# Kernel optimization log

Measured on AMD Instinct MI355X. Metric: run time of the kernel, lower is better.

Reference implementation:

```python
import jax, jax.numpy as jnp
import numpy as np

H, DK, DV = 16, 64, 64


def _ln(x, w, b, eps=1e-5):
    mu = x.mean(-1, keepdims=True)
    var = ((x - mu) ** 2).mean(-1, keepdims=True)
    return (x - mu) * jax.lax.rsqrt(var + eps) * w + b


def setup_inputs() -> dict:
    key = jax.random.key(0)
    ks = jax.random.split(key, 8)
    B, L, D = 4, 1024, 1024
    q = jax.random.normal(ks[0], (B, L, D), jnp.float32)
    k = jax.random.normal(ks[1], (B, L, D), jnp.float32)
    v = jax.random.normal(ks[2], (B, L, D), jnp.float32)
    mask = jax.random.randint(ks[3], (B, L, L), 0, 2).astype(jnp.int32)
    diag_mask = jnp.zeros((1,), jnp.int32)  # unused by the original attention math
    sq = np.sqrt(2.0 / (D + DK)).astype(np.float32)
    sv = np.sqrt(2.0 / (D + DV)).astype(np.float32)
    wq = jax.random.normal(ks[4], (H * DK, D), jnp.float32) * sq
    wk = jax.random.normal(ks[5], (H * DK, D), jnp.float32) * sq
    wv = jax.random.normal(ks[6], (H * DV, D), jnp.float32) * sv
    wfc = jax.random.normal(ks[7], (D, H * DV), jnp.float32) * 0.02
    ones, zeros = jnp.ones((D,), jnp.float32), jnp.zeros((D,), jnp.float32)
    return {
        'q': q, 'k': k, 'v': v, 'diag_mask': diag_mask, 'mask': mask,
        'ln1_w': ones, 'ln1_b': zeros, 'ln2_w': ones, 'ln2_b': zeros,
        'ln3_w': ones, 'ln3_b': zeros, 'wq': wq, 'wk': wk, 'wv': wv, 'wfc': wfc,
    }


def reference(q, k, v, diag_mask, mask, ln1_w, ln1_b, ln2_w, ln2_b, ln3_w, ln3_b, wq, wk, wv, wfc):
    B, Lq, _ = q.shape
    Lk = k.shape[1]
    qn = _ln(q, ln1_w, ln1_b)
    kn = _ln(k, ln2_w, ln2_b)
    vn = _ln(v, ln3_w, ln3_b)
    qh = (qn @ wq.T).reshape(B, Lq, H, DK)
    kh = (kn @ wk.T).reshape(B, Lk, H, DK)
    vh = (vn @ wv.T).reshape(B, Lk, H, DV)
    # head-major layout matches torch's permute(2,0,1,3).view(-1,...)
    logits = jnp.einsum('bqhd,bkhd->hbqk', qh, kh) / jnp.float32(DK ** 0.5)
    m = mask[None] != 0  # broadcast mask over heads, [1,B,Lq,Lk]
    logits = jnp.where(m, jnp.float32(-1e32), logits)  # memory_efficient mask_fill
    p = jax.nn.softmax(logits, axis=-1)
    p = p * (~m)  # post-softmax zeroing, as in masked_softmax
    ctx = jnp.einsum('hbqk,bkhd->bqhd', p, vh).reshape(B, Lq, H * DV)
    dynamic = ctx @ wfc.T  # fc1: single bias-free Linear, no tanh/dropout
    attn = p.reshape(H * B, Lq, Lk)
    return dynamic, attn
```

## Files before the change

### kernel.cpp

```cpp
#include <hip/hip_runtime.h>
#include <hip/hip_bf16.h>

#define B_ 4
#define L_ 1024
#define D_ 1024
#define H_ 16
#define NROWS_ (B_ * L_)

typedef __attribute__((ext_vector_type(8))) short short8;
typedef __attribute__((ext_vector_type(4))) float f32x4;

__device__ __forceinline__ ushort f2bf(float f) {
    union { float f; uint u; } x; x.f = f;
    return (ushort)((x.u + 0x7fffu + ((x.u >> 16) & 1u)) >> 16);
}
__device__ __forceinline__ float bf2f(ushort u) {
    union { uint u; float f; } x; x.u = (uint)u << 16; return x.f;
}
__device__ __forceinline__ void gl_lds16(const void* g, void* l) {
    __builtin_amdgcn_global_load_lds(
        (const __attribute__((address_space(1))) uint*)(uintptr_t)g,
        (__attribute__((address_space(3))) uint*)(uintptr_t)l, 16, 0, 0);
}

#define EXP2C 0.1803368801111244f

__global__ __launch_bounds__(256) void lnwcvt_kernel(
    const float* __restrict__ q, const float* __restrict__ k, const float* __restrict__ v,
    const float* __restrict__ ln1w, const float* __restrict__ ln1b,
    const float* __restrict__ ln2w, const float* __restrict__ ln2b,
    const float* __restrict__ ln3w, const float* __restrict__ ln3b,
    ushort* __restrict__ qn, ushort* __restrict__ kn, ushort* __restrict__ vn,
    const float* __restrict__ wq, const float* __restrict__ wk,
    const float* __restrict__ wv, const float* __restrict__ wfc,
    ushort* __restrict__ wqb, ushort* __restrict__ wkb,
    ushort* __restrict__ wvb, ushort* __restrict__ wfcb)
{
    const int bid = blockIdx.x, t = threadIdx.x;
    if (bid >= 12288) {
        const int wbid = bid - 12288;
        const int which = wbid >> 10;
        const float* src = which == 0 ? wq : which == 1 ? wk : which == 2 ? wv : wfc;
        ushort* dst      = which == 0 ? wqb : which == 1 ? wkb : which == 2 ? wvb : wfcb;
        const size_t i = (size_t)(wbid & 1023) * 256 + t;
        const float4 f = ((const float4*)src)[i];
        ushort4 o; o.x = f2bf(f.x); o.y = f2bf(f.y); o.z = f2bf(f.z); o.w = f2bf(f.w);
        ((ushort4*)dst)[i] = o;
        return;
    }
    const int which = bid >> 12, row = bid & 4095;
    const float *x, *lw, *lb; ushort* out;
    if (which == 0)      { x = q; lw = ln1w; lb = ln1b; out = qn; }
    else if (which == 1) { x = k; lw = ln2w; lb = ln2b; out = kn; }
    else                 { x = v; lw = ln3w; lb = ln3b; out = vn; }
    x += (size_t)row * D_; out += (size_t)row * D_;
    const float4 t4 = ((const float4*)x)[t];
    float s  = t4.x + t4.y + t4.z + t4.w;
    float s2 = t4.x*t4.x + t4.y*t4.y + t4.z*t4.z + t4.w*t4.w;
    #pragma unroll
    for (int off = 1; off < 64; off <<= 1) {
        s  += __shfl_xor(s,  off, 64);
        s2 += __shfl_xor(s2, off, 64);
    }
    __shared__ float red[8];
    __shared__ float mr[2];
    const int wid = t >> 6;
    if ((t & 63) == 0) { red[wid*2] = s; red[wid*2+1] = s2; }
    __syncthreads();
    if (t == 0) {
        s  = red[0] + red[2] + red[4] + red[6];
        s2 = red[1] + red[3] + red[5] + red[7];
        const float mean = s * (1.0f/(float)D_);
        const float var  = s2 * (1.0f/(float)D_) - mean*mean;
        mr[0] = mean; mr[1] = rsqrtf(var + 1e-5f);
    }
    __syncthreads();
    const float mean = mr[0], rstd = mr[1];
    const float4 w4 = ((const float4*)lw)[t];
    const float4 b4 = ((const float4*)lb)[t];
    ushort4 o;
    o.x = f2bf((t4.x - mean)*rstd*w4.x + b4.x);
    o.y = f2bf((t4.y - mean)*rstd*w4.y + b4.y);
    o.z = f2bf((t4.z - mean)*rstd*w4.z + b4.z);
    o.w = f2bf((t4.w - mean)*rstd*w4.w + b4.w);
    ((ushort4*)out)[t] = o;
}

__global__ __launch_bounds__(256) void projgather_kernel(
    const ushort* __restrict__ qn, const ushort* __restrict__ kn, const ushort* __restrict__ vn,
    const ushort* __restrict__ wqb, const ushort* __restrict__ wkb, const ushort* __restrict__ wvb,
    ushort* __restrict__ qh, ushort* __restrict__ kh, ushort* __restrict__ vtw,
    const int* __restrict__ mask, uint2* __restrict__ gbits)
{
    const int gid = blockIdx.x;
    const int t = threadIdx.x;
    if (gid >= 768) {
        const int row = (gid - 768) * 16 + (t >> 4);
        const int lc = t & 15;
        const int* src = mask + (size_t)row * 1024 + lc;
        uint lo = 0, hi = 0;
        #pragma unroll
        for (int j = 0; j < 32; j++) lo |= (__builtin_nontemporal_load(&src[16*j])      != 0 ? 1u : 0u) << j;
        #pragma unroll
        for (int j = 0; j < 32; j++) hi |= (__builtin_nontemporal_load(&src[16*(j+32)]) != 0 ? 1u : 0u) << j;
        gbits[(size_t)row*16 + lc] = make_uint2(lo, hi);
        return;
    }
    __shared__ __align__(16) ushort As[128*64];
    __shared__ __align__(16) ushort Bs[128*64];
    const int z = gid % 3, id = gid / 3;
    const ushort *A, *W; ushort* out;
    if (z == 0)      { A = qn;  W = wqb; out = qh;  }
    else if (z == 1) { A = kn;  W = wkb; out = kh;  }
    else             { A = wvb; W = vn;  out = vtw; }
    int bm, bn;
    if (z < 2) { bm = (id >> 3) * 128; bn = (id & 7)  * 128; }
    else       { bm = (id >> 5) * 128; bn = (id & 31) * 128; }

    const int w = t >> 6, lane = t & 63;
    const int lc = lane & 15, g = lane >> 4;
    const int wr = w >> 1, wc = w & 1;
    const int srow = lane >> 3, sp = lane & 7;
    f32x4 acc[4][4] = {};

    for (int k0 = 0; k0 < 1024; k0 += 64) {
        #pragma unroll
        for (int j = 0; j < 4; j++) {
            const int i = w*4 + j;
            const int row = i*8 + srow;
            const int c = (sp - (row & 7)) & 7;
            gl_lds16(A + (size_t)(bm+row)*1024 + k0 + c*8, &As[i*512]);
            gl_lds16(W + (size_t)(bn+row)*1024 + k0 + c*8, &Bs[i*512]);
        }
        __syncthreads();
        #pragma unroll
        for (int ks = 0; ks < 2; ks++) {
            short8 af[4], bf4[4];
            #pragma unroll
            for (int mi = 0; mi < 4; mi++) {
                const int row = wr*64 + mi*16 + lc;
                af[mi] = *(const short8*)&As[row*64 + (((ks*4+g) + (row&7)) & 7)*8];
            }
            #pragma unroll
            for (int ni = 0; ni < 4; ni++) {
                const int row = wc*64 + ni*16 + lc;
                bf4[ni] = *(const short8*)&Bs[row*64 + (((ks*4+g) + (row&7)) & 7)*8];
            }
            #pragma unroll
            for (int mi = 0; mi < 4; mi++)
                #pragma unroll
                for (int ni = 0; ni < 4; ni++)
                    acc[mi][ni] = __builtin_amdgcn_mfma_f32_16x16x32_bf16(af[mi], bf4[ni], acc[mi][ni], 0, 0, 0);
        }
        __syncthreads();
    }

    const float scale = (z == 0) ? EXP2C : 1.0f;
    #pragma unroll
    for (int mi = 0; mi < 4; mi++)
        #pragma unroll
        for (int ni = 0; ni < 4; ni++)
            #pragma unroll
            for (int r = 0; r < 4; r++) {
                const int m = bm + wr*64 + mi*16 + g*4 + r;
                const int n = bn + wc*64 + ni*16 + lc;
                const ushort val = f2bf(acc[mi][ni][r] * scale);
                if (z < 2) {
                    const int bb = m >> 10, seq = m & 1023, hh = n >> 6, d = n & 63;
                    out[(((size_t)(bb*16+hh))*1024 + seq)*64 + d] = val;
                } else {
                    const int bb = n >> 10, seq = n & 1023, hh = m >> 6, d = m & 63;
                    out[((size_t)(bb*16+hh))*65536 + (size_t)d*1024 + seq] = val;
                }
            }
}

__global__ __launch_bounds__(256) void fc_kernel(
    const ushort* __restrict__ A, const ushort* __restrict__ W, float* __restrict__ C)
{
    __shared__ __align__(16) ushort As[128*64];
    __shared__ __align__(16) ushort Bs[64*64];
    const int t = threadIdx.x, w = t >> 6, lane = t & 63;
    const int lc = lane & 15, g = lane >> 4;
    const int wr = w >> 1, wc = w & 1;
    const int bm = blockIdx.x * 128, bn = blockIdx.y * 64;
    const int srow = lane >> 3, sp = lane & 7;
    f32x4 acc[4][2] = {};

    for (int k0 = 0; k0 < 1024; k0 += 64) {
        #pragma unroll
        for (int j = 0; j < 4; j++) {
            const int i = w*4 + j;
            const int row = i*8 + srow;
            const int c = (sp - (row & 7)) & 7;
            gl_lds16(A + (size_t)(bm+row)*1024 + k0 + c*8, &As[i*512]);
        }
        #pragma unroll
        for (int j = 0; j < 2; j++) {
            const int i = w*2 + j;
            const int row = i*8 + srow;
            const int c = (sp - (row & 7)) & 7;
            gl_lds16(W + (size_t)(bn+row)*1024 + k0 + c*8, &Bs[i*512]);
        }
        __syncthreads();
        #pragma unroll
        for (int ks = 0; ks < 2; ks++) {
            short8 af[4], bf4[2];
            #pragma unroll
            for (int mi = 0; mi < 4; mi++) {
                const int row = wr*64 + mi*16 + lc;
                af[mi] = *(const short8*)&As[row*64 + (((ks*4+g) + (row&7)) & 7)*8];
            }
            #pragma unroll
            for (int ni = 0; ni < 2; ni++) {
                const int row = wc*32 + ni*16 + lc;
                bf4[ni] = *(const short8*)&Bs[row*64 + (((ks*4+g) + (row&7)) & 7)*8];
            }
            #pragma unroll
            for (int mi = 0; mi < 4; mi++)
                #pragma unroll
                for (int ni = 0; ni < 2; ni++)
                    acc[mi][ni] = __builtin_amdgcn_mfma_f32_16x16x32_bf16(af[mi], bf4[ni], acc[mi][ni], 0, 0, 0);
        }
        __syncthreads();
    }

    #pragma unroll
    for (int mi = 0; mi < 4; mi++)
        #pragma unroll
        for (int ni = 0; ni < 2; ni++)
            #pragma unroll
            for (int r = 0; r < 4; r++)
                C[(size_t)(bm + wr*64 + mi*16 + g*4 + r)*1024 + bn + wc*32 + ni*16 + lc] = acc[mi][ni][r];
}

#define AS_VMCNT(N) asm volatile("s_waitcnt vmcnt(" #N ")" ::: "memory")
#define AS_BAR()    asm volatile("s_barrier" ::: "memory")

__global__ __launch_bounds__(256, 3) void attn_kernel(
    const ushort* __restrict__ qh, const ushort* __restrict__ kh, const ushort* __restrict__ vt,
    const uint2* __restrict__ gbits, float* __restrict__ p_out, ushort* __restrict__ ctx)
{
    __shared__ __align__(16) ushort KV[4][64*64];
    __shared__ __align__(16) ushort Pb[4][16*72];
    const int t = threadIdx.x, w = t >> 6, lane = t & 63;
    const int lc = lane & 15, g = lane >> 4;
    const int q0 = blockIdx.x * 64, h = blockIdx.y, b = blockIdx.z;
    const int qrow = w * 16;
    const ushort* qbase = qh + ((size_t)(b*16+h)*1024 + q0 + qrow)*64;
    const ushort* kbase = kh + (size_t)(b*16+h)*1024*64;
    const ushort* vbase = vt + (size_t)(b*16+h)*64*1024;
    ushort* PbW = Pb[w];

    const short8 aq0 = *(const short8*)(qbase + (size_t)lc*64 + g*8);
    const short8 aq1 = *(const short8*)(qbase + (size_t)lc*64 + 32 + g*8);

    unsigned long long gb[4];
    #pragma unroll
    for (int r = 0; r < 4; r++) {
        const uint2 u = gbits[((size_t)(b*1024 + q0 + qrow + g*4 + r))*16 + lc];
        gb[r] = ((unsigned long long)u.y << 32) | (unsigned long long)u.x;
    }

    const int rsub = lane >> 3, sp = lane & 7;
    const int c = (sp - rsub) & 7;
    const int r0 = w*16 + rsub, r1 = w*16 + 8 + rsub;

    gl_lds16(kbase + (size_t)r0*64 + c*8,            &KV[0][(w*2+0)*512]);
    gl_lds16(kbase + (size_t)r1*64 + c*8,            &KV[0][(w*2+1)*512]);
    gl_lds16(kbase + (size_t)(64+r0)*64 + c*8,       &KV[1][(w*2+0)*512]);
    gl_lds16(kbase + (size_t)(64+r1)*64 + c*8,       &KV[1][(w*2+1)*512]);

    float s_part[4] = {0.f, 0.f, 0.f, 0.f};

    for (int kt = 0; kt < 16; kt++) {
        const ushort* kcur = KV[kt % 3];
        if (kt < 14) {
            ushort* dst = KV[(kt + 2) % 3];
            gl_lds16(kbase + ((size_t)((kt+2)*64+r0))*64 + c*8, &dst[(w*2+0)*512]);
            gl_lds16(kbase + ((size_t)((kt+2)*64+r1))*64 + c*8, &dst[(w*2+1)*512]);
            AS_VMCNT(4);
        } else if (kt == 14) {
            AS_VMCNT(2);
        } else {
            AS_VMCNT(0);
        }
        AS_BAR();
        f32x4 sacc[4];
        __builtin_amdgcn_s_setprio(1);
        #pragma unroll
        for (int ni = 0; ni < 4; ni++) {
            const int row = ni*16 + lc;
            const short8 b0 = *(const short8*)&kcur[row*64 + (((g  ) + (row&7)) & 7)*8];
            const short8 b1 = *(const short8*)&kcur[row*64 + (((4+g) + (row&7)) & 7)*8];
            f32x4 z = {0.f,0.f,0.f,0.f};
            z = __builtin_amdgcn_mfma_f32_16x16x32_bf16(aq0, b0, z, 0, 0, 0);
            z = __builtin_amdgcn_mfma_f32_16x16x32_bf16(aq1, b1, z, 0, 0, 0);
            sacc[ni] = z;
        }
        __builtin_amdgcn_s_setprio(0);
        #pragma unroll
        for (int r = 0; r < 4; r++)
            #pragma unroll
            for (int ni = 0; ni < 4; ni++) {
                const bool mk = (gb[r] >> (kt*4 + ni)) & 1ull;
                s_part[r] += mk ? 0.f : exp2f(sacc[ni][r]);
            }
        AS_BAR();
    }

    gl_lds16(kbase + (size_t)r0*64 + c*8,    &KV[0][(w*2+0)*512]);
    gl_lds16(kbase + (size_t)r1*64 + c*8,    &KV[0][(w*2+1)*512]);
    gl_lds16(vbase + (size_t)r0*1024 + c*8,  &KV[2][(w*2+0)*512]);
    gl_lds16(vbase + (size_t)r1*1024 + c*8,  &KV[2][(w*2+1)*512]);

    float inv[4];
    #pragma unroll
    for (int r = 0; r < 4; r++) {
        float s = s_part[r];
        #pragma unroll
        for (int off = 1; off < 16; off <<= 1) s += __shfl_xor(s, off, 64);
        inv[r] = (s > 0.f) ? (1.0f / s) : 0.f;
    }

    f32x4 cacc[4] = {{0,0,0,0},{0,0,0,0},{0,0,0,0},{0,0,0,0}};
    float* pblk = p_out + ((size_t)(h*B_ + b)*1024 + q0 + qrow)*1024;
    for (int kt = 0; kt < 16; kt++) {
        const int cur = kt & 1;
        if (kt < 15) {
            gl_lds16(kbase + ((size_t)((kt+1)*64+r0))*64 + c*8,   &KV[cur^1][(w*2+0)*512]);
            gl_lds16(kbase + ((size_t)((kt+1)*64+r1))*64 + c*8,   &KV[cur^1][(w*2+1)*512]);
            gl_lds16(vbase + (size_t)r0*1024 + (kt+1)*64 + c*8,   &KV[2+(cur^1)][(w*2+0)*512]);
            gl_lds16(vbase + (size_t)r1*1024 + (kt+1)*64 + c*8,   &KV[2+(cur^1)][(w*2+1)*512]);
        }
        if (kt == 0 || kt == 15) { AS_VMCNT(4); } else { AS_VMCNT(8); }
        AS_BAR();
        const ushort* kcur = KV[cur];
        const ushort* vcur = KV[2 + cur];
        f32x4 sacc[4];
        __builtin_amdgcn_s_setprio(1);
        #pragma unroll
        for (int ni = 0; ni < 4; ni++) {
            const int row = ni*16 + lc;
            const short8 b0 = *(const short8*)&kcur[row*64 + (((g  ) + (row&7)) & 7)*8];
            const short8 b1 = *(const short8*)&kcur[row*64 + (((4+g) + (row&7)) & 7)*8];
            f32x4 z = {0.f,0.f,0.f,0.f};
            z = __builtin_amdgcn_mfma_f32_16x16x32_bf16(aq0, b0, z, 0, 0, 0);
            z = __builtin_amdgcn_mfma_f32_16x16x32_bf16(aq1, b1, z, 0, 0, 0);
            sacc[ni] = z;
        }
        __builtin_amdgcn_s_setprio(0);
        #pragma unroll
        for (int r = 0; r < 4; r++)
            #pragma unroll
            for (int ni = 0; ni < 4; ni++) {
                const bool mk = (gb[r] >> (kt*4 + ni)) & 1ull;
                const float pn = mk ? 0.f : exp2f(sacc[ni][r]) * inv[r];
                PbW[(g*4+r)*72 + ni*16 + lc] = f2bf(pn);
            }
        {
            const int rr = lane >> 2, c4 = (lane & 3) * 16;
            const short8 e0 = *(const short8*)&PbW[rr*72 + c4 + 0];
            const short8 e1 = *(const short8*)&PbW[rr*72 + c4 + 8];
            float* dst = pblk + (size_t)rr*1024 + kt*64 + c4;
            float4 o;
            o.x = bf2f((ushort)e0[0]); o.y = bf2f((ushort)e0[1]);
            o.z = bf2f((ushort)e0[2]); o.w = bf2f((ushort)e0[3]);
            *(float4*)(dst + 0) = o;
            o.x = bf2f((ushort)e0[4]); o.y = bf2f((ushort)e0[5]);
            o.z = bf2f((ushort)e0[6]); o.w = bf2f((ushort)e0[7]);
            *(float4*)(dst + 4) = o;
            o.x = bf2f((ushort)e1[0]); o.y = bf2f((ushort)e1[1]);
            o.z = bf2f((ushort)e1[2]); o.w = bf2f((ushort)e1[3]);
            *(float4*)(dst + 8) = o;
            o.x = bf2f((ushort)e1[4]); o.y = bf2f((ushort)e1[5]);
            o.z = bf2f((ushort)e1[6]); o.w = bf2f((ushort)e1[7]);
            *(float4*)(dst + 12) = o;
        }
        const short8 pa0 = *(const short8*)&PbW[lc*72 + g*8];
        const short8 pa1 = *(const short8*)&PbW[lc*72 + 32 + g*8];
        __builtin_amdgcn_s_setprio(1);
        #pragma unroll
        for (int di = 0; di < 4; di++) {
            const int row = di*16 + lc;
            const short8 vb0 = *(const short8*)&vcur[row*64 + (((g  ) + (row&7)) & 7)*8];
            const short8 vb1 = *(const short8*)&vcur[row*64 + (((4+g) + (row&7)) & 7)*8];
            cacc[di] = __builtin_amdgcn_mfma_f32_16x16x32_bf16(pa0, vb0, cacc[di], 0, 0, 0);
            cacc[di] = __builtin_amdgcn_mfma_f32_16x16x32_bf16(pa1, vb1, cacc[di], 0, 0, 0);
        }
        __builtin_amdgcn_s_setprio(0);
        AS_BAR();
    }

    #pragma unroll
    for (int di = 0; di < 4; di++)
        #pragma unroll
        for (int r = 0; r < 4; r++)
            PbW[(g*4+r)*72 + di*16 + lc] = f2bf(cacc[di][r]);
    {
        const int rr = lane >> 2, seg = (lane & 3) * 16;
        const short8 c0 = *(const short8*)&PbW[rr*72 + seg + 0];
        const short8 c1 = *(const short8*)&PbW[rr*72 + seg + 8];
        ushort* dst = ctx + ((size_t)(b*1024 + q0 + qrow + rr))*1024 + h*64 + seg;
        *(short8*)(dst + 0) = c0;
        *(short8*)(dst + 8) = c1;
    }
}

extern "C" void kernel_launch(void* const* d_in, const int* in_sizes, int n_in,
                              void* d_out, int out_size, void* d_ws, size_t ws_size,
                              hipStream_t stream)
{
    const float* q    = (const float*)d_in[0];
    const float* k    = (const float*)d_in[1];
    const float* v    = (const float*)d_in[2];
    const int*   mask = (const int*)d_in[4];
    const float* ln1w = (const float*)d_in[5];
    const float* ln1b = (const float*)d_in[6];
    const float* ln2w = (const float*)d_in[7];
    const float* ln2b = (const float*)d_in[8];
    const float* ln3w = (const float*)d_in[9];
    const float* ln3b = (const float*)d_in[10];
    const float* wq   = (const float*)d_in[11];
    const float* wk   = (const float*)d_in[12];
    const float* wv   = (const float*)d_in[13];
    const float* wfc  = (const float*)d_in[14];

    float* dyn_out  = (float*)d_out;
    float* attn_out = dyn_out + (size_t)B_ * L_ * D_;

    char* ws = (char*)d_ws;
    uint2*  gbits = (uint2*)ws;       ws += (size_t)NROWS_ * 16 * 8;
    ushort* qn    = (ushort*)ws;      ws += (size_t)NROWS_ * D_ * 2;
    ushort* kn    = (ushort*)ws;      ws += (size_t)NROWS_ * D_ * 2;
    ushort* vn    = (ushort*)ws;      ws += (size_t)NROWS_ * D_ * 2;
    ushort* wqb   = (ushort*)ws;      ws += (size_t)D_ * D_ * 2;
    ushort* wkb   = (ushort*)ws;      ws += (size_t)D_ * D_ * 2;
    ushort* wvb   = (ushort*)ws;      ws += (size_t)D_ * D_ * 2;
    ushort* wfcb  = (ushort*)ws;      ws += (size_t)D_ * D_ * 2;
    ushort* qh    = (ushort*)ws;      ws += (size_t)NROWS_ * D_ * 2;
    ushort* kh    = (ushort*)ws;      ws += (size_t)NROWS_ * D_ * 2;
    ushort* vtw   = (ushort*)ws;      ws += (size_t)NROWS_ * D_ * 2;
    ushort* ctx   = qn;

    lnwcvt_kernel<<<16384, 256, 0, stream>>>(q, k, v, ln1w, ln1b, ln2w, ln2b, ln3w, ln3b,
                                             qn, kn, vn, wq, wk, wv, wfc, wqb, wkb, wvb, wfcb);

    projgather_kernel<<<1024, 256, 0, stream>>>(qn, kn, vn, wqb, wkb, wvb, qh, kh, vtw, mask, gbits);

    attn_kernel<<<dim3(16, 16, 4), 256, 0, stream>>>(qh, kh, vtw, gbits, attn_out, ctx);

    fc_kernel<<<dim3(32, 16), 256, 0, stream>>>(ctx, wfcb, dyn_out);
}
```

Baseline: 209.0 us.

## Widen attention blocks to 128 query rows with 8 waves sharing K/V tiles

Doubles the attention block's query tile from 64 to 128 rows by using 512 threads (8 waves), so each K/V tile staged in LDS is reused by twice as many waves. Each thread now issues one global-to-LDS load per tile instead of two, and the vmcnt waits are recomputed for the new per-thread load counts. This halves redundant K/V global traffic per head but halves the grid size and changes occupancy (launch bounds 512,2), which risks fewer resident waves and less latency hiding.

Measured after the change: 204.9 us. About the same (-1.9%).

```diff
diff --git a/kernel.cpp b/kernel.cpp
--- a/kernel.cpp
+++ b/kernel.cpp
@@ -237,15 +237,15 @@
 #define AS_VMCNT(N) asm volatile("s_waitcnt vmcnt(" #N ")" ::: "memory")
 #define AS_BAR()    asm volatile("s_barrier" ::: "memory")
 
-__global__ __launch_bounds__(256, 3) void attn_kernel(
+__global__ __launch_bounds__(512, 2) void attn_kernel(
     const ushort* __restrict__ qh, const ushort* __restrict__ kh, const ushort* __restrict__ vt,
     const uint2* __restrict__ gbits, float* __restrict__ p_out, ushort* __restrict__ ctx)
 {
     __shared__ __align__(16) ushort KV[4][64*64];
-    __shared__ __align__(16) ushort Pb[4][16*72];
+    __shared__ __align__(16) ushort Pb[8][16*72];
     const int t = threadIdx.x, w = t >> 6, lane = t & 63;
     const int lc = lane & 15, g = lane >> 4;
-    const int q0 = blockIdx.x * 64, h = blockIdx.y, b = blockIdx.z;
+    const int q0 = blockIdx.x * 128, h = blockIdx.y, b = blockIdx.z;
     const int qrow = w * 16;
     const ushort* qbase = qh + ((size_t)(b*16+h)*1024 + q0 + qrow)*64;
     const ushort* kbase = kh + (size_t)(b*16+h)*1024*64;
@@ -262,26 +262,22 @@
         gb[r] = ((unsigned long long)u.y << 32) | (unsigned long long)u.x;
     }
 
-    const int rsub = lane >> 3, sp = lane & 7;
-    const int c = (sp - rsub) & 7;
-    const int r0 = w*16 + rsub, r1 = w*16 + 8 + rsub;
-
-    gl_lds16(kbase + (size_t)r0*64 + c*8,            &KV[0][(w*2+0)*512]);
-    gl_lds16(kbase + (size_t)r1*64 + c*8,            &KV[0][(w*2+1)*512]);
-    gl_lds16(kbase + (size_t)(64+r0)*64 + c*8,       &KV[1][(w*2+0)*512]);
-    gl_lds16(kbase + (size_t)(64+r1)*64 + c*8,       &KV[1][(w*2+1)*512]);
+    const int srow = t >> 3;
+    const int sp = t & 7;
+    const int c = (sp - (srow & 7)) & 7;
+
+    gl_lds16(kbase + (size_t)srow*64 + c*8,        &KV[0][w*512]);
+    gl_lds16(kbase + (size_t)(64+srow)*64 + c*8,   &KV[1][w*512]);
 
     float s_part[4] = {0.f, 0.f, 0.f, 0.f};
 
     for (int kt = 0; kt < 16; kt++) {
         const ushort* kcur = KV[kt % 3];
         if (kt < 14) {
-            ushort* dst = KV[(kt + 2) % 3];
-            gl_lds16(kbase + ((size_t)((kt+2)*64+r0))*64 + c*8, &dst[(w*2+0)*512]);
-            gl_lds16(kbase + ((size_t)((kt+2)*64+r1))*64 + c*8, &dst[(w*2+1)*512]);
-            AS_VMCNT(4);
+            gl_lds16(kbase + ((size_t)((kt+2)*64+srow))*64 + c*8, &KV[(kt+2)%3][w*512]);
+            AS_VMCNT(2);
         } else if (kt == 14) {
-            AS_VMCNT(2);
+            AS_VMCNT(1);
         } else {
             AS_VMCNT(0);
         }
@@ -309,10 +305,8 @@
         AS_BAR();
     }
 
-    gl_lds16(kbase + (size_t)r0*64 + c*8,    &KV[0][(w*2+0)*512]);
-    gl_lds16(kbase + (size_t)r1*64 + c*8,    &KV[0][(w*2+1)*512]);
-    gl_lds16(vbase + (size_t)r0*1024 + c*8,  &KV[2][(w*2+0)*512]);
-    gl_lds16(vbase + (size_t)r1*1024 + c*8,  &KV[2][(w*2+1)*512]);
+    gl_lds16(kbase + (size_t)srow*64 + c*8,    &KV[0][w*512]);
+    gl_lds16(vbase + (size_t)srow*1024 + c*8,  &KV[2][w*512]);
 
     float inv[4];
     #pragma unroll
@@ -328,12 +322,10 @@
     for (int kt = 0; kt < 16; kt++) {
         const int cur = kt & 1;
         if (kt < 15) {
-            gl_lds16(kbase + ((size_t)((kt+1)*64+r0))*64 + c*8,   &KV[cur^1][(w*2+0)*512]);
-            gl_lds16(kbase + ((size_t)((kt+1)*64+r1))*64 + c*8,   &KV[cur^1][(w*2+1)*512]);
-            gl_lds16(vbase + (size_t)r0*1024 + (kt+1)*64 + c*8,   &KV[2+(cur^1)][(w*2+0)*512]);
-            gl_lds16(vbase + (size_t)r1*1024 + (kt+1)*64 + c*8,   &KV[2+(cur^1)][(w*2+1)*512]);
-        }
-        if (kt == 0 || kt == 15) { AS_VMCNT(4); } else { AS_VMCNT(8); }
+            gl_lds16(kbase + ((size_t)((kt+1)*64+srow))*64 + c*8, &KV[cur^1][w*512]);
+            gl_lds16(vbase + (size_t)srow*1024 + (kt+1)*64 + c*8, &KV[2+(cur^1)][w*512]);
+        }
+        if (kt == 0) { AS_VMCNT(2); } else if (kt == 15) { AS_VMCNT(4); } else { AS_VMCNT(6); }
         AS_BAR();
         const ushort* kcur = KV[cur];
         const ushort* vcur = KV[2 + cur];
@@ -448,7 +440,7 @@
 
     projgather_kernel<<<1024, 256, 0, stream>>>(qn, kn, vn, wqb, wkb, wvb, qh, kh, vtw, mask, gbits);
 
-    attn_kernel<<<dim3(16, 16, 4), 256, 0, stream>>>(qh, kh, vtw, gbits, attn_out, ctx);
+    attn_kernel<<<dim3(8, 16, 4), 512, 0, stream>>>(qh, kh, vtw, gbits, attn_out, ctx);
 
     fc_kernel<<<dim3(32, 16), 256, 0, stream>>>(ctx, wfcb, dyn_out);
 }
```
